# Kernel tuning notes

Hardware: AMD Instinct MI355X
Metric: run time of the kernel (lower is better)

Reference implementation:

```python
import jax, jax.numpy as jnp
import numpy as np

N = 8192
D_IN = 32
HIDDEN = [32, 32, 32]   # -> 2 GraphConvolution layers
FC = [32, 1]            # hfc = [32, 32, 1] -> 2 Linear layers


def _uniform(key, shape, stdv):
    return jax.random.uniform(key, shape, jnp.float32, -stdv, stdv)


def setup_inputs() -> dict:
    key = jax.random.key(0)
    ks = jax.random.split(key, 32)
    inp = {}
    inp["V"] = jax.random.normal(ks[0], (N, D_IN), jnp.float32)
    inp["adj"] = jax.random.randint(ks[1], (N, N), 0, 4, jnp.int32)
    # GCN layer params: w1, w2, w3 [in, out], bias [out]; init U(-stdv, stdv), stdv = 1/sqrt(out)
    ki = 2
    for li in range(len(HIDDEN) - 1):
        a, b = HIDDEN[li], HIDDEN[li + 1]
        stdv = 1.0 / np.sqrt(b)
        for wname in ("w1", "w2", "w3"):
            inp[f"{wname}_{li}"] = _uniform(ks[ki], (a, b), stdv); ki += 1
        inp[f"gb_{li}"] = _uniform(ks[ki], (b,), stdv); ki += 1
    # FC params (torch Linear default init: U(-1/sqrt(in), 1/sqrt(in)))
    hfc = [HIDDEN[-1]] + FC
    for li in range(len(hfc) - 1):
        a, b = hfc[li], hfc[li + 1]
        stdv = 1.0 / np.sqrt(a)
        inp[f"fcW_{li}"] = _uniform(ks[ki], (b, a), stdv); ki += 1  # torch Linear weight is [out, in]
        inp[f"fcb_{li}"] = _uniform(ks[ki], (b,), stdv); ki += 1
    return inp


def _gcn(V, adj, w1, w2, w3, bias):
    # masked-adjacency relational aggregation: sum_k (adj==k) @ (V @ w_k)
    dt = V.dtype
    o = (adj == 1).astype(dt) @ (V @ w1)
    o = o + (adj == 2).astype(dt) @ (V @ w2)
    o = o + (adj == 3).astype(dt) @ (V @ w3)
    return jax.nn.relu(o + bias)


def reference(V, adj, w1_0, w2_0, w3_0, gb_0, w1_1, w2_1, w3_1, gb_1,
              fcW_0, fcb_0, fcW_1, fcb_1):
    Z = _gcn(V, adj, w1_0, w2_0, w3_0, gb_0)          # [N, 32]
    Z = _gcn(Z, adj, w1_1, w2_1, w3_1, gb_1)          # [N, 32]
    Z = jnp.sum(Z, axis=0)                             # [32] sum pooling over nodes
    Z = jax.nn.relu(Z @ fcW_0.T + fcb_0)               # dropout = identity (eval mode)
    Z = Z @ fcW_1.T + fcb_1                            # [1]
    return jax.nn.sigmoid(Z)
```

## Files before the change

### kernel.cpp

```cpp
#include <hip/hip_runtime.h>
#include <cmath>

#define NN 8192

typedef _Float16 half8 __attribute__((ext_vector_type(8)));
typedef float floatx4 __attribute__((ext_vector_type(4)));
typedef unsigned int uint;

template <int L2>
__global__ __launch_bounds__(256) void h_kernel(
    const float* __restrict__ X, const float* __restrict__ w1,
    const float* __restrict__ w2, const float* __restrict__ w3,
    const float* __restrict__ gbias, _Float16* __restrict__ Hfrag) {
  __shared__ float wl[32][32];
  __shared__ float Xs[64][32];
  const int tid = threadIdx.x;
  const int ch = blockIdx.y;
  const float* wsrc = (ch == 0) ? w1 : (ch == 1) ? w2 : w3;
  for (int i = tid; i < 1024; i += 256) ((float*)wl)[i] = wsrc[i];
  const size_t base = (size_t)blockIdx.x * 2048 + tid * 8;
  if (L2 == 0) {
    float4 x0 = ((const float4*)(X + base))[0];
    float4 x1 = ((const float4*)(X + base))[1];
    *((float4*)(&Xs[0][0] + tid * 8)) = x0;
    *((float4*)(&Xs[0][0] + tid * 8 + 4)) = x1;
  } else {
    float4 s0 = {0.f, 0.f, 0.f, 0.f}, s1 = {0.f, 0.f, 0.f, 0.f};
#pragma unroll
    for (int c = 0; c < 8; ++c) {
      const float4* p = (const float4*)(X + (size_t)c * NN * 32 + base);
      float4 a = p[0], b = p[1];
      s0.x += a.x; s0.y += a.y; s0.z += a.z; s0.w += a.w;
      s1.x += b.x; s1.y += b.y; s1.z += b.z; s1.w += b.w;
    }
    const int c0 = (tid * 8) & 31;
    const float4 b0 = *(const float4*)(gbias + c0);
    const float4 b1 = *(const float4*)(gbias + c0 + 4);
    s0.x += b0.x; s0.y += b0.y; s0.z += b0.z; s0.w += b0.w;
    s1.x += b1.x; s1.y += b1.y; s1.z += b1.z; s1.w += b1.w;
    s0.x = s0.x > 0.f ? s0.x : 0.f; s0.y = s0.y > 0.f ? s0.y : 0.f;
    s0.z = s0.z > 0.f ? s0.z : 0.f; s0.w = s0.w > 0.f ? s0.w : 0.f;
    s1.x = s1.x > 0.f ? s1.x : 0.f; s1.y = s1.y > 0.f ? s1.y : 0.f;
    s1.z = s1.z > 0.f ? s1.z : 0.f; s1.w = s1.w > 0.f ? s1.w : 0.f;
    *((float4*)(&Xs[0][0] + tid * 8)) = s0;
    *((float4*)(&Xs[0][0] + tid * 8 + 4)) = s1;
  }
  __syncthreads();
  const int n = tid & 31, jb = tid >> 5;
  const int j0 = blockIdx.x * 64 + jb * 8;
  const int t = j0 >> 5;
  const int lane = (n & 15) | (((j0 & 31) >> 3) << 4);
  const int tile = n >> 4;
  half8 hv;
#pragma unroll
  for (int jj = 0; jj < 8; ++jj) {
    const float4* xr = (const float4*)(&Xs[jb * 8 + jj][0]);
    float acc = 0.f;
#pragma unroll
    for (int d4 = 0; d4 < 8; ++d4) {
      float4 x = xr[d4];
      acc += x.x * wl[d4 * 4 + 0][n];
      acc += x.y * wl[d4 * 4 + 1][n];
      acc += x.z * wl[d4 * 4 + 2][n];
      acc += x.w * wl[d4 * 4 + 3][n];
    }
    hv[jj] = (_Float16)acc;
  }
  size_t idx = ((((size_t)ch * 256 + t) * 2 + tile) * 64 + lane) * 8;
  *(half8*)(Hfrag + idx) = hv;
}

__device__ __forceinline__ void phaseB_core(const uint* mk,
                                            const half8* __restrict__ Hf,
                                            float* red_raw,
                                            float* __restrict__ Zpart, int rg,
                                            int c, int tid) {
  const int w = tid >> 6, lane = tid & 63;
  const int m = lane & 15, q = lane >> 4;
  const half8* hp = Hf + (size_t)(c * 32 + w * 8) * 128 + lane;
  half8 b00 = hp[0],     b01 = hp[64];
  half8 b10 = hp[32768], b11 = hp[32768 + 64];
  half8 b20 = hp[65536], b21 = hp[65536 + 64];
  floatx4 acc00 = {0.f, 0.f, 0.f, 0.f}, acc01 = {0.f, 0.f, 0.f, 0.f};
  floatx4 acc10 = {0.f, 0.f, 0.f, 0.f}, acc11 = {0.f, 0.f, 0.f, 0.f};
#pragma unroll
  for (int tl = 0; tl < 8; ++tl) {
    half8 n00, n01, n10, n11, n20, n21;
    if (tl < 7) {
      const half8* np = hp + (tl + 1) * 128;
      n00 = np[0];     n01 = np[64];
      n10 = np[32768]; n11 = np[32768 + 64];
      n20 = np[65536]; n21 = np[65536 + 64];
    }
    const uint pk = mk[tl];
    half8 a1r0, a2r0, a3r0, a1r1, a2r1, a3r1;
#pragma unroll
    for (int i = 0; i < 8; ++i) {
      const int p0 = (pk >> (2 * i)) & 3;
      const int p1 = (pk >> (16 + 2 * i)) & 3;
      a1r0[i] = (p0 == 1) ? (_Float16)1.f : (_Float16)0.f;
      a2r0[i] = (p0 == 2) ? (_Float16)1.f : (_Float16)0.f;
      a3r0[i] = (p0 == 3) ? (_Float16)1.f : (_Float16)0.f;
      a1r1[i] = (p1 == 1) ? (_Float16)1.f : (_Float16)0.f;
      a2r1[i] = (p1 == 2) ? (_Float16)1.f : (_Float16)0.f;
      a3r1[i] = (p1 == 3) ? (_Float16)1.f : (_Float16)0.f;
    }
    acc00 = __builtin_amdgcn_mfma_f32_16x16x32_f16(a1r0, b00, acc00, 0, 0, 0);
    acc00 = __builtin_amdgcn_mfma_f32_16x16x32_f16(a2r0, b10, acc00, 0, 0, 0);
    acc00 = __builtin_amdgcn_mfma_f32_16x16x32_f16(a3r0, b20, acc00, 0, 0, 0);
    acc01 = __builtin_amdgcn_mfma_f32_16x16x32_f16(a1r0, b01, acc01, 0, 0, 0);
    acc01 = __builtin_amdgcn_mfma_f32_16x16x32_f16(a2r0, b11, acc01, 0, 0, 0);
    acc01 = __builtin_amdgcn_mfma_f32_16x16x32_f16(a3r0, b21, acc01, 0, 0, 0);
    acc10 = __builtin_amdgcn_mfma_f32_16x16x32_f16(a1r1, b00, acc10, 0, 0, 0);
    acc10 = __builtin_amdgcn_mfma_f32_16x16x32_f16(a2r1, b10, acc10, 0, 0, 0);
    acc10 = __builtin_amdgcn_mfma_f32_16x16x32_f16(a3r1, b20, acc10, 0, 0, 0);
    acc11 = __builtin_amdgcn_mfma_f32_16x16x32_f16(a1r1, b01, acc11, 0, 0, 0);
    acc11 = __builtin_amdgcn_mfma_f32_16x16x32_f16(a2r1, b11, acc11, 0, 0, 0);
    acc11 = __builtin_amdgcn_mfma_f32_16x16x32_f16(a3r1, b21, acc11, 0, 0, 0);
    if (tl < 7) {
      b00 = n00; b01 = n01; b10 = n10; b11 = n11; b20 = n20; b21 = n21;
    }
  }
  float (*red)[4][64][4] = (float (*)[4][64][4])red_raw;
#pragma unroll
  for (int r = 0; r < 4; ++r) {
    red[w][0][lane][r] = acc00[r];
    red[w][1][lane][r] = acc01[r];
    red[w][2][lane][r] = acc10[r];
    red[w][3][lane][r] = acc11[r];
  }
  __syncthreads();
  if (w == 0) {
    const int rbase = rg * 32;
#pragma unroll
    for (int r = 0; r < 4; ++r) {
      const float c00 = red[0][0][lane][r] + red[1][0][lane][r] +
                        red[2][0][lane][r] + red[3][0][lane][r];
      const float c01 = red[0][1][lane][r] + red[1][1][lane][r] +
                        red[2][1][lane][r] + red[3][1][lane][r];
      const float c10 = red[0][2][lane][r] + red[1][2][lane][r] +
                        red[2][2][lane][r] + red[3][2][lane][r];
      const float c11 = red[0][3][lane][r] + red[1][3][lane][r] +
                        red[2][3][lane][r] + red[3][3][lane][r];
      const int ro0 = rbase + q * 4 + r;
      float* zp0 = Zpart + ((size_t)c * NN + ro0) * 32;
      zp0[m] = c00;
      zp0[16 + m] = c01;
      float* zp1 = Zpart + ((size_t)c * NN + ro0 + 16) * 32;
      zp1[m] = c10;
      zp1[16 + m] = c11;
    }
  }
}

__global__ __launch_bounds__(256, 4) void agg1_kernel(
    const int* __restrict__ adj, uint* __restrict__ packed_g,
    const half8* __restrict__ Hf, float* __restrict__ Zpart) {
  __shared__ char smraw[16384];
  uint* ptile = (uint*)smraw;
  const int tid = threadIdx.x;
  const int rg = blockIdx.x >> 3, c = blockIdx.x & 7;
  const int tg = tid >> 5;
  const int qt = (tid >> 1) & 3;
  const int t4 = (tid >> 3) & 3;
  const int ih = tid & 1;
  const int byte_base = tg * 1024 + qt * 256 + t4 * 4 + ih;
  unsigned char* pb = (unsigned char*)ptile;
  const size_t gofs = (size_t)rg * 32 * NN + c * 1024 + tid * 4;
#pragma unroll
  for (int r0 = 0; r0 < 32; r0 += 8) {
    int4 a[8];
#pragma unroll
    for (int rr = 0; rr < 8; ++rr)
      a[rr] = *(const int4*)(adj + gofs + (size_t)(r0 + rr) * NN);
#pragma unroll
    for (int rr = 0; rr < 8; ++rr) {
      const int r = r0 + rr;
      const uint b = (uint)(a[rr].x & 3) | ((uint)(a[rr].y & 3) << 2) |
                     ((uint)(a[rr].z & 3) << 4) | ((uint)(a[rr].w & 3) << 6);
      pb[byte_base + (r & 15) * 16 + (r >> 4) * 2] = (unsigned char)b;
    }
  }
  __syncthreads();
  uint* pg = packed_g + (size_t)blockIdx.x * 2048;
  *(uint4*)(pg + tid * 8) = *(const uint4*)(ptile + tid * 8);
  *(uint4*)(pg + tid * 8 + 4) = *(const uint4*)(ptile + tid * 8 + 4);
  const int w = tid >> 6, lane = tid & 63;
  uint mk[8];
  *(uint4*)(mk) = *(const uint4*)(ptile + (w * 2) * 256 + lane * 4);
  *(uint4*)(mk + 4) = *(const uint4*)(ptile + (w * 2 + 1) * 256 + lane * 4);
  __syncthreads();
  phaseB_core(mk, Hf, (float*)smraw, Zpart, rg, c, tid);
}

__global__ __launch_bounds__(256, 4) void agg2_kernel(
    const uint* __restrict__ packed_g, const half8* __restrict__ Hf,
    float* __restrict__ Zpart) {
  __shared__ float red_lds[4][4][64][4];
  const int tid = threadIdx.x;
  const int rg = blockIdx.x >> 3, c = blockIdx.x & 7;
  const int w = tid >> 6, lane = tid & 63;
  const uint* pg =
      packed_g + (size_t)blockIdx.x * 2048 + (w * 2) * 256 + lane * 4;
  uint mk[8];
  *(uint4*)(mk) = *(const uint4*)(pg);
  *(uint4*)(mk + 4) = *(const uint4*)(pg + 256);
  phaseB_core(mk, Hf, (float*)red_lds, Zpart, rg, c, tid);
}

__global__ __launch_bounds__(256) void pool_kernel(
    const float* __restrict__ Zpart, const float* __restrict__ bias,
    float* __restrict__ partials) {
  const int tid = threadIdx.x;
  const int col = tid & 31, ro = tid >> 5;
  const float b = bias[col];
  float s = 0.f;
  for (int rr = 0; rr < 32; ++rr) {
    const size_t r = (size_t)blockIdx.x * 256 + ro * 32 + rr;
    float v = b;
#pragma unroll
    for (int c = 0; c < 8; ++c) v += Zpart[(size_t)c * NN * 32 + r * 32 + col];
    s += v > 0.f ? v : 0.f;
  }
  __shared__ float red[8][32];
  red[ro][col] = s;
  __syncthreads();
  if (tid < 32) {
    float t = 0.f;
#pragma unroll
    for (int i = 0; i < 8; ++i) t += red[i][tid];
    partials[(size_t)blockIdx.x * 32 + tid] = t;
  }
}

__global__ __launch_bounds__(256) void fc_kernel(
    const float* __restrict__ partials, int np, const float* __restrict__ W0,
    const float* __restrict__ b0, const float* __restrict__ W1,
    const float* __restrict__ b1, float* __restrict__ out) {
  __shared__ float acc8[8][32];
  __shared__ float z[32], y[32];
  const int tid = threadIdx.x;
  const int col = tid & 31, ch = tid >> 5;
  float s = 0.f;
  for (int i = ch; i < np; i += 8) s += partials[(size_t)i * 32 + col];
  acc8[ch][col] = s;
  __syncthreads();
  if (tid < 32) {
    float t = 0.f;
#pragma unroll
    for (int i = 0; i < 8; ++i) t += acc8[i][tid];
    z[tid] = t;
  }
  __syncthreads();
  if (tid < 32) {
    float acc = b0[tid];
    for (int n = 0; n < 32; ++n) acc += W0[tid * 32 + n] * z[n];
    y[tid] = acc > 0.f ? acc : 0.f;
  }
  __syncthreads();
  if (tid == 0) {
    float acc = b1[0];
    for (int mm = 0; mm < 32; ++mm) acc += W1[mm] * y[mm];
    out[0] = 1.f / (1.f + expf(-acc));
  }
}

extern "C" void kernel_launch(void* const* d_in, const int* in_sizes, int n_in,
                              void* d_out, int out_size, void* d_ws,
                              size_t ws_size, hipStream_t stream) {
  const float* V   = (const float*)d_in[0];
  const int*   adj = (const int*)d_in[1];
  const float *w10 = (const float*)d_in[2], *w20 = (const float*)d_in[3],
              *w30 = (const float*)d_in[4], *gb0 = (const float*)d_in[5];
  const float *w11 = (const float*)d_in[6], *w21 = (const float*)d_in[7],
              *w31 = (const float*)d_in[8], *gb1 = (const float*)d_in[9];
  const float *fW0 = (const float*)d_in[10], *fb0 = (const float*)d_in[11],
              *fW1 = (const float*)d_in[12], *fb1 = (const float*)d_in[13];
  float* out = (float*)d_out;
  char* ws = (char*)d_ws;

  _Float16* Hfrag    = (_Float16*)ws;
  float*    Zpart    = (float*)(ws + 1572864);
  float*    partials = (float*)(ws + 9961472);
  uint*     packed   = (uint*)(ws + 10223616);

  h_kernel<0><<<dim3(128, 3), 256, 0, stream>>>(V, w10, w20, w30, nullptr,
                                                Hfrag);
  agg1_kernel<<<2048, 256, 0, stream>>>(adj, packed, (const half8*)Hfrag,
                                        Zpart);
  h_kernel<1><<<dim3(128, 3), 256, 0, stream>>>(Zpart, w11, w21, w31, gb0,
                                                Hfrag);
  agg2_kernel<<<2048, 256, 0, stream>>>(packed, (const half8*)Hfrag, Zpart);
  pool_kernel<<<32, 256, 0, stream>>>(Zpart, gb1, partials);
  fc_kernel<<<1, 256, 0, stream>>>(partials, 32, fW0, fb0, fW1, fb1, out);
}
```

Measured before the change: 439.1 us.

## Switch aggregation MFMAs to FP8 with bit-trick mask construction

The H fragments are now quantized to FP8 (e4m3) instead of FP16, and the aggregation uses the 16x16x32 fp8 MFMA. The one-hot adjacency masks are built with packed bit arithmetic that emits the FP8 byte 0x40 (the value 2.0), replacing per-element selects. The result is scaled by 0.5 to compensate. This halves H load traffic and cuts the VALU work of mask construction, and it targets the higher FP8 matrix throughput. The cost is FP8 quantization error on the intermediate features, which may threaten numerical tolerance.

```diff
diff --git a/kernel.cpp b/kernel.cpp
--- a/kernel.cpp
+++ b/kernel.cpp
@@ -3,15 +3,15 @@
 
 #define NN 8192
 
-typedef _Float16 half8 __attribute__((ext_vector_type(8)));
 typedef float floatx4 __attribute__((ext_vector_type(4)));
 typedef unsigned int uint;
+typedef unsigned long long u64;
 
 template <int L2>
 __global__ __launch_bounds__(256) void h_kernel(
     const float* __restrict__ X, const float* __restrict__ w1,
     const float* __restrict__ w2, const float* __restrict__ w3,
-    const float* __restrict__ gbias, _Float16* __restrict__ Hfrag) {
+    const float* __restrict__ gbias, u64* __restrict__ Hfrag) {
   __shared__ float wl[32][32];
   __shared__ float Xs[64][32];
   const int tid = threadIdx.x;
@@ -51,7 +51,7 @@
   const int t = j0 >> 5;
   const int lane = (n & 15) | (((j0 & 31) >> 3) << 4);
   const int tile = n >> 4;
-  half8 hv;
+  float av[8];
 #pragma unroll
   for (int jj = 0; jj < 8; ++jj) {
     const float4* xr = (const float4*)(&Xs[jb * 8 + jj][0]);
@@ -64,59 +64,76 @@
       acc += x.z * wl[d4 * 4 + 2][n];
       acc += x.w * wl[d4 * 4 + 3][n];
     }
-    hv[jj] = (_Float16)acc;
-  }
-  size_t idx = ((((size_t)ch * 256 + t) * 2 + tile) * 64 + lane) * 8;
-  *(half8*)(Hfrag + idx) = hv;
-}
+    av[jj] = acc;
+  }
+  int lo = __builtin_amdgcn_cvt_pk_fp8_f32(av[0], av[1], 0, false);
+  lo = __builtin_amdgcn_cvt_pk_fp8_f32(av[2], av[3], lo, true);
+  int hi = __builtin_amdgcn_cvt_pk_fp8_f32(av[4], av[5], 0, false);
+  hi = __builtin_amdgcn_cvt_pk_fp8_f32(av[6], av[7], hi, true);
+  size_t idx = (((size_t)ch * 256 + t) * 2 + tile) * 64 + lane;
+  Hfrag[idx] = ((u64)(uint)hi << 32) | (uint)(uint)lo;
+}
+
+#define BUILD_MASK(z, r0out, r1out)                                       \
+  {                                                                       \
+    const uint d0 = ((((z) & 0x55u) * 0x41041u) & 0x01010101u) << 6;      \
+    const uint d1 = (((((z) >> 8) & 0x55u) * 0x41041u) & 0x01010101u)     \
+                    << 6;                                                 \
+    const uint d2 = (((((z) >> 16) & 0x55u) * 0x41041u) & 0x01010101u)    \
+                    << 6;                                                 \
+    const uint d3 = (((((z) >> 24) & 0x55u) * 0x41041u) & 0x01010101u)    \
+                    << 6;                                                 \
+    r0out = (long long)(((u64)d1 << 32) | d0);                            \
+    r1out = (long long)(((u64)d3 << 32) | d2);                            \
+  }
+
+#define MF8(A, B, C) __builtin_amdgcn_mfma_f32_16x16x32_fp8_fp8((A), (B), (C), 0, 0, 0)
 
 __device__ __forceinline__ void phaseB_core(const uint* mk,
-                                            const half8* __restrict__ Hf,
+                                            const u64* __restrict__ Hf,
                                             float* red_raw,
                                             float* __restrict__ Zpart, int rg,
                                             int c, int tid) {
   const int w = tid >> 6, lane = tid & 63;
   const int m = lane & 15, q = lane >> 4;
-  const half8* hp = Hf + (size_t)(c * 32 + w * 8) * 128 + lane;
-  half8 b00 = hp[0],     b01 = hp[64];
-  half8 b10 = hp[32768], b11 = hp[32768 + 64];
-  half8 b20 = hp[65536], b21 = hp[65536 + 64];
+  const u64* hp = Hf + (size_t)(c * 32 + w * 8) * 128 + lane;
+  long long b00 = hp[0],     b01 = hp[64];
+  long long b10 = hp[32768], b11 = hp[32768 + 64];
+  long long b20 = hp[65536], b21 = hp[65536 + 64];
   floatx4 acc00 = {0.f, 0.f, 0.f, 0.f}, acc01 = {0.f, 0.f, 0.f, 0.f};
   floatx4 acc10 = {0.f, 0.f, 0.f, 0.f}, acc11 = {0.f, 0.f, 0.f, 0.f};
 #pragma unroll
   for (int tl = 0; tl < 8; ++tl) {
-    half8 n00, n01, n10, n11, n20, n21;
+    long long n00, n01, n10, n11, n20, n21;
     if (tl < 7) {
-      const half8* np = hp + (tl + 1) * 128;
+      const u64* np = hp + (tl + 1) * 128;
       n00 = np[0];     n01 = np[64];
       n10 = np[32768]; n11 = np[32768 + 64];
       n20 = np[65536]; n21 = np[65536 + 64];
     }
     const uint pk = mk[tl];
-    half8 a1r0, a2r0, a3r0, a1r1, a2r1, a3r1;
-#pragma unroll
-    for (int i = 0; i < 8; ++i) {
-      const int p0 = (pk >> (2 * i)) & 3;
-      const int p1 = (pk >> (16 + 2 * i)) & 3;
-      a1r0[i] = (p0 == 1) ? (_Float16)1.f : (_Float16)0.f;
-      a2r0[i] = (p0 == 2) ? (_Float16)1.f : (_Float16)0.f;
-      a3r0[i] = (p0 == 3) ? (_Float16)1.f : (_Float16)0.f;
-      a1r1[i] = (p1 == 1) ? (_Float16)1.f : (_Float16)0.f;
-      a2r1[i] = (p1 == 2) ? (_Float16)1.f : (_Float16)0.f;
-      a3r1[i] = (p1 == 3) ? (_Float16)1.f : (_Float16)0.f;
-    }
-    acc00 = __builtin_amdgcn_mfma_f32_16x16x32_f16(a1r0, b00, acc00, 0, 0, 0);
-    acc00 = __builtin_amdgcn_mfma_f32_16x16x32_f16(a2r0, b10, acc00, 0, 0, 0);
-    acc00 = __builtin_amdgcn_mfma_f32_16x16x32_f16(a3r0, b20, acc00, 0, 0, 0);
-    acc01 = __builtin_amdgcn_mfma_f32_16x16x32_f16(a1r0, b01, acc01, 0, 0, 0);
-    acc01 = __builtin_amdgcn_mfma_f32_16x16x32_f16(a2r0, b11, acc01, 0, 0, 0);
-    acc01 = __builtin_amdgcn_mfma_f32_16x16x32_f16(a3r0, b21, acc01, 0, 0, 0);
-    acc10 = __builtin_amdgcn_mfma_f32_16x16x32_f16(a1r1, b00, acc10, 0, 0, 0);
-    acc10 = __builtin_amdgcn_mfma_f32_16x16x32_f16(a2r1, b10, acc10, 0, 0, 0);
-    acc10 = __builtin_amdgcn_mfma_f32_16x16x32_f16(a3r1, b20, acc10, 0, 0, 0);
-    acc11 = __builtin_amdgcn_mfma_f32_16x16x32_f16(a1r1, b01, acc11, 0, 0, 0);
-    acc11 = __builtin_amdgcn_mfma_f32_16x16x32_f16(a2r1, b11, acc11, 0, 0, 0);
-    acc11 = __builtin_amdgcn_mfma_f32_16x16x32_f16(a3r1, b21, acc11, 0, 0, 0);
+    const uint x1 = pk ^ 0x55555555u;
+    const uint z1 = ~(x1 | (x1 >> 1)) & 0x55555555u;
+    const uint x2 = pk ^ 0xAAAAAAAAu;
+    const uint z2 = ~(x2 | (x2 >> 1)) & 0x55555555u;
+    const uint x3 = ~pk;
+    const uint z3 = ~(x3 | (x3 >> 1)) & 0x55555555u;
+    long long a1r0, a1r1, a2r0, a2r1, a3r0, a3r1;
+    BUILD_MASK(z1, a1r0, a1r1);
+    BUILD_MASK(z2, a2r0, a2r1);
+    BUILD_MASK(z3, a3r0, a3r1);
+    acc00 = MF8(a1r0, b00, acc00);
+    acc00 = MF8(a2r0, b10, acc00);
+    acc00 = MF8(a3r0, b20, acc00);
+    acc01 = MF8(a1r0, b01, acc01);
+    acc01 = MF8(a2r0, b11, acc01);
+    acc01 = MF8(a3r0, b21, acc01);
+    acc10 = MF8(a1r1, b00, acc10);
+    acc10 = MF8(a2r1, b10, acc10);
+    acc10 = MF8(a3r1, b20, acc10);
+    acc11 = MF8(a1r1, b01, acc11);
+    acc11 = MF8(a2r1, b11, acc11);
+    acc11 = MF8(a3r1, b21, acc11);
     if (tl < 7) {
       b00 = n00; b01 = n01; b10 = n10; b11 = n11; b20 = n20; b21 = n21;
     }
@@ -134,14 +151,14 @@
     const int rbase = rg * 32;
 #pragma unroll
     for (int r = 0; r < 4; ++r) {
-      const float c00 = red[0][0][lane][r] + red[1][0][lane][r] +
-                        red[2][0][lane][r] + red[3][0][lane][r];
-      const float c01 = red[0][1][lane][r] + red[1][1][lane][r] +
-                        red[2][1][lane][r] + red[3][1][lane][r];
-      const float c10 = red[0][2][lane][r] + red[1][2][lane][r] +
-                        red[2][2][lane][r] + red[3][2][lane][r];
-      const float c11 = red[0][3][lane][r] + red[1][3][lane][r] +
-                        red[2][3][lane][r] + red[3][3][lane][r];
+      const float c00 = 0.5f * (red[0][0][lane][r] + red[1][0][lane][r] +
+                                red[2][0][lane][r] + red[3][0][lane][r]);
+      const float c01 = 0.5f * (red[0][1][lane][r] + red[1][1][lane][r] +
+                                red[2][1][lane][r] + red[3][1][lane][r]);
+      const float c10 = 0.5f * (red[0][2][lane][r] + red[1][2][lane][r] +
+                                red[2][2][lane][r] + red[3][2][lane][r]);
+      const float c11 = 0.5f * (red[0][3][lane][r] + red[1][3][lane][r] +
+                                red[2][3][lane][r] + red[3][3][lane][r]);
       const int ro0 = rbase + q * 4 + r;
       float* zp0 = Zpart + ((size_t)c * NN + ro0) * 32;
       zp0[m] = c00;
@@ -155,7 +172,7 @@
 
 __global__ __launch_bounds__(256, 4) void agg1_kernel(
     const int* __restrict__ adj, uint* __restrict__ packed_g,
-    const half8* __restrict__ Hf, float* __restrict__ Zpart) {
+    const u64* __restrict__ Hf, float* __restrict__ Zpart) {
   __shared__ char smraw[16384];
   uint* ptile = (uint*)smraw;
   const int tid = threadIdx.x;
@@ -194,7 +211,7 @@
 }
 
 __global__ __launch_bounds__(256, 4) void agg2_kernel(
-    const uint* __restrict__ packed_g, const half8* __restrict__ Hf,
+    const uint* __restrict__ packed_g, const u64* __restrict__ Hf,
     float* __restrict__ Zpart) {
   __shared__ float red_lds[4][4][64][4];
   const int tid = threadIdx.x;
@@ -279,18 +296,17 @@
   float* out = (float*)d_out;
   char* ws = (char*)d_ws;
 
-  _Float16* Hfrag    = (_Float16*)ws;
-  float*    Zpart    = (float*)(ws + 1572864);
-  float*    partials = (float*)(ws + 9961472);
-  uint*     packed   = (uint*)(ws + 10223616);
+  u64*   Hfrag    = (u64*)ws;
+  float* Zpart    = (float*)(ws + 786432);
+  float* partials = (float*)(ws + 9175040);
+  uint*  packed   = (uint*)(ws + 9437184);
 
   h_kernel<0><<<dim3(128, 3), 256, 0, stream>>>(V, w10, w20, w30, nullptr,
                                                 Hfrag);
-  agg1_kernel<<<2048, 256, 0, stream>>>(adj, packed, (const half8*)Hfrag,
-                                        Zpart);
+  agg1_kernel<<<2048, 256, 0, stream>>>(adj, packed, Hfrag, Zpart);
   h_kernel<1><<<dim3(128, 3), 256, 0, stream>>>(Zpart, w11, w21, w31, gb0,
                                                 Hfrag);
-  agg2_kernel<<<2048, 256, 0, stream>>>(packed, (const half8*)Hfrag, Zpart);
+  agg2_kernel<<<2048, 256, 0, stream>>>(packed, Hfrag, Zpart);
   pool_kernel<<<32, 256, 0, stream>>>(Zpart, gb1, partials);
   fc_kernel<<<1, 256, 0, stream>>>(partials, 32, fW0, fb0, fW1, fb1, out);
 }
```

New measurement: 421.7 us. -3.9%, faster.
